# Optimization experiments

Measured on AMD Instinct MI355X. Metric: run time of the kernel, lower is better.

The kernel has to match this reference:

```python
import jax, jax.numpy as jnp
import numpy as np

H = W = 1024
CHUNK = 32  # rows per chunk in the column EDT pass (keeps intermediate at 32*H*W floats)


def setup_inputs() -> dict:
    key = jax.random.key(0)
    k1, k2 = jax.random.split(key)
    preds = jax.random.randint(k1, (H, W), 0, 2).astype(jnp.float32)
    targets = jax.random.randint(k2, (H, W), 0, 2).astype(jnp.float32)
    return {"preds": preds, "targets": targets}


def _edges(seg):
    # morphological erosion via 3x3 box conv, threshold at 9 == kernel.numel()
    s = seg[None, None]  # (1,1,H,W)
    kern = jnp.ones((1, 1, 3, 3), seg.dtype)
    conv = jax.lax.conv_general_dilated(s, kern, (1, 1), ((1, 1), (1, 1)))
    eroded = (conv[0, 0] == 9.0).astype(seg.dtype)
    return seg - eroded


def _edt(edges):
    # exact Euclidean distance transform: distance to nearest zero of (1 - edges),
    # i.e. nearest pixel where edges == 1.  Separable exact algorithm:
    #   1) per-row 1D distance to nearest feature (via cummax/cummin scans)
    #   2) per-column lower envelope min_k g2[k,j] + (i-k)^2 (chunked brute force)
    feat = (1.0 - edges) == 0.0
    Hh, Ww = edges.shape
    BIG = jnp.float32(1e6)
    col = jnp.arange(Ww, dtype=jnp.float32)
    left = col - jax.lax.cummax(jnp.where(feat, col, -BIG), axis=1)
    right = jax.lax.cummin(jnp.where(feat, col, BIG), axis=1, reverse=True) - col
    g = jnp.minimum(jnp.minimum(left, right), BIG)  # row-wise 1D distance
    g2 = g * g  # (H,W) squared row distances
    rows = jnp.arange(Hh, dtype=jnp.float32)

    def chunk(ic):  # ic: (CHUNK,) target row indices
        # (CHUNK, H, W): g2[k,j] + (i-k)^2, min over source row k
        d = g2[None, :, :] + (ic[:, None, None] - rows[None, :, None]) ** 2
        return jnp.min(d, axis=1)  # (CHUNK, W)

    D2 = jax.lax.map(chunk, rows.reshape(-1, CHUNK)).reshape(Hh, Ww)
    return jnp.sqrt(D2)


def reference(preds, targets):
    pred_edges = _edges(preds)
    target_edges = _edges(targets)
    # scipy EDT ran on detached CPU copies -> no gradient through the DTs
    pred_dt = jax.lax.stop_gradient(_edt(pred_edges))
    target_dt = jax.lax.stop_gradient(_edt(target_edges))
    pred_err = target_edges * pred_dt
    target_err = pred_edges * target_dt
    loss = (jnp.mean(pred_err) + jnp.mean(target_err)) / 2.0
    return jax.nn.sigmoid(loss)
```

## Files before the change

kernel.cpp:

```cpp
#include <hip/hip_runtime.h>
#include <hip/hip_bf16.h>
#include <math.h>


#define HW 1024
#define BIGF 1e6f
#define RMIN_SENT (1 << 30)

__global__ __launch_bounds__(256)
void k_rows(const float* __restrict__ pred, const float* __restrict__ targ,
            float* __restrict__ hp, float* __restrict__ ht,
            unsigned char* __restrict__ ep, unsigned char* __restrict__ et)
{
    const int r = blockIdx.x;
    const int m = blockIdx.y;
    const int t = threadIdx.x;
    const float* __restrict__ seg = m ? targ : pred;
    float* __restrict__ hout = m ? ht : hp;
    unsigned char* __restrict__ eout = m ? et : ep;

    __shared__ unsigned char colall[HW];
    __shared__ int wtotL[4];
    __shared__ int wtotR[4];

    const int j4 = t * 4;
    float4 c0 = *(const float4*)&seg[r * HW + j4];
    float4 cm = make_float4(0.f, 0.f, 0.f, 0.f);
    float4 cp = make_float4(0.f, 0.f, 0.f, 0.f);
    if (r > 0)        cm = *(const float4*)&seg[(r - 1) * HW + j4];
    if (r < HW - 1)   cp = *(const float4*)&seg[(r + 1) * HW + j4];

    const float s0v[4] = {c0.x, c0.y, c0.z, c0.w};
    const float smv[4] = {cm.x, cm.y, cm.z, cm.w};
    const float spv[4] = {cp.x, cp.y, cp.z, cp.w};

    unsigned char ca[4];
    #pragma unroll
    for (int u = 0; u < 4; ++u)
        ca[u] = (s0v[u] != 0.f && smv[u] != 0.f && spv[u] != 0.f) ? 1 : 0;
    *(uchar4*)&colall[j4] = make_uchar4(ca[0], ca[1], ca[2], ca[3]);
    __syncthreads();

    int lmax = -1, rmin = RMIN_SENT;
    unsigned char fe[4];
    #pragma unroll
    for (int u = 0; u < 4; ++u) {
        const int j = j4 + u;
        int er = 0;
        if (j > 0 && j < HW - 1)
            er = colall[j - 1] & ca[u] & colall[j + 1];
        const int e = (s0v[u] != 0.f) && !er;
        fe[u] = (unsigned char)e;
        if (e) { lmax = j; if (rmin == RMIN_SENT) rmin = j; }
    }
    *(uchar4*)&eout[r * HW + j4] = make_uchar4(fe[0], fe[1], fe[2], fe[3]);

    const int lane = t & 63;
    const int wv   = t >> 6;
    int Li = lmax;
    #pragma unroll
    for (int off = 1; off < 64; off <<= 1) {
        const int v = __shfl_up(Li, off);
        if (lane >= off) Li = max(Li, v);
    }
    int Ri = rmin;
    #pragma unroll
    for (int off = 1; off < 64; off <<= 1) {
        const int v = __shfl_down(Ri, off);
        if (lane + off < 64) Ri = min(Ri, v);
    }
    if (lane == 63) wtotL[wv] = Li;
    if (lane == 0)  wtotR[wv] = Ri;
    int exL = __shfl_up(Li, 1);  if (lane == 0)  exL = -1;
    int exR = __shfl_down(Ri, 1); if (lane == 63) exR = RMIN_SENT;
    __syncthreads();
    int baseL = -1, baseR = RMIN_SENT;
    #pragma unroll
    for (int w2 = 0; w2 < 4; ++w2) {
        if (w2 < wv) baseL = max(baseL, wtotL[w2]);
        if (w2 > wv) baseR = min(baseR, wtotR[w2]);
    }
    const int carryL = max(baseL, exL);
    const int carryR = min(baseR, exR);

    int Lv[4], Rv[4];
    {
        int L = carryL;
        #pragma unroll
        for (int u = 0; u < 4; ++u) { if (fe[u]) L = j4 + u; Lv[u] = L; }
    }
    {
        int R = carryR;
        #pragma unroll
        for (int u = 3; u >= 0; --u) { if (fe[u]) R = j4 + u; Rv[u] = R; }
    }

    const float rr = (float)(r * r);
    float hv[4];
    #pragma unroll
    for (int u = 0; u < 4; ++u) {
        const float jf = (float)(j4 + u);
        const float left  = jf - ((Lv[u] < 0) ? -BIGF : (float)Lv[u]);
        const float right = ((Rv[u] >= RMIN_SENT) ? BIGF : (float)Rv[u]) - jf;
        float g = fminf(fminf(left, right), BIGF);
        hv[u] = g * g + rr;
    }
    float4 ho; ho.x = hv[0]; ho.y = hv[1]; ho.z = hv[2]; ho.w = hv[3];
    *(float4*)&hout[r * HW + j4] = ho;
}

#define WIN 8
#define RPB 128
#define KROWS (RPB + 2 * WIN)
#define HS_STRIDE 17
#define NBLK 1024

__global__ __launch_bounds__(256)
void k_cols(const float* __restrict__ hp, const float* __restrict__ ht,
            const unsigned char* __restrict__ ep, const unsigned char* __restrict__ et,
            float* __restrict__ partial)
{
    const int j0 = blockIdx.x * 16;
    const int i0 = blockIdx.y * RPB;
    const int m  = blockIdx.z;
    const float* __restrict__ hg = m ? ht : hp;
    const unsigned char* __restrict__ ew = m ? ep : et;

    __shared__ float hs[KROWS * HS_STRIDE];
    __shared__ alignas(16) unsigned char es[RPB * 16];
    __shared__ float wsum[4];

    for (int idx = threadIdx.x; idx < KROWS * 16; idx += 256) {
        const int kk = idx >> 4, jc = idx & 15;
        const int gk = i0 - WIN + kk;
        float v = 1e30f;
        if ((unsigned)gk < (unsigned)HW) v = hg[gk * HW + j0 + jc];
        hs[kk * HS_STRIDE + jc] = v;
    }
    if (threadIdx.x < RPB)
        *(uint4*)&es[threadIdx.x * 16] = *(const uint4*)&ew[(i0 + threadIdx.x) * HW + j0];
    __syncthreads();

    const int jj = threadIdx.x & 15;
    const int iw = threadIdx.x >> 4;
    float lsum = 0.f;

    #pragma unroll
    for (int g = 0; g < 2; ++g) {
        const int ib = i0 + iw * 8 + g * 4;
        const int kkS = iw * 8 + g * 4;
        float b0 = 3e38f, b1 = 3e38f, b2 = 3e38f, b3 = 3e38f;
        float kf = (float)(ib - WIN);
        const float m0 = -2.f * (float)(ib);
        const float m1 = -2.f * (float)(ib + 1);
        const float m2 = -2.f * (float)(ib + 2);
        const float m3 = -2.f * (float)(ib + 3);
        #pragma unroll
        for (int kk = kkS; kk < kkS + 2 * WIN + 4; ++kk) {
            const float hvv = hs[kk * HS_STRIDE + jj];
            b0 = fminf(b0, fmaf(m0, kf, hvv));
            b1 = fminf(b1, fmaf(m1, kf, hvv));
            b2 = fminf(b2, fmaf(m2, kf, hvv));
            b3 = fminf(b3, fmaf(m3, kf, hvv));
            kf += 1.f;
        }
        const int sLo = max(0, ib - WIN);
        const int sHi = min(HW - 1, ib + WIN + 3);
        float bs[4] = {b0, b1, b2, b3};
        #pragma unroll
        for (int w = 0; w < 4; ++w) {
            const int i = ib + w;
            float D2 = (float)(i * i) + bs[w];
            const int dl = i - sLo + 1, dr = sHi + 1 - i;
            const bool need = ((sLo > 0) && (D2 > (float)(dl * dl))) ||
                              ((sHi < HW - 1) && (D2 > (float)(dr * dr)));
            if (need) {
                float bb = 3e38f, k2 = 0.f;
                const float mm = -2.f * (float)i;
                for (int k = 0; k < HW; ++k) {
                    bb = fminf(bb, fmaf(mm, k2, hg[k * HW + j0 + jj]));
                    k2 += 1.f;
                }
                D2 = (float)(i * i) + bb;
            }
            const float wgt = (float)es[(i - i0) * 16 + jj];
            lsum = fmaf(wgt, sqrtf(D2), lsum);
        }
    }

    #pragma unroll
    for (int off = 32; off > 0; off >>= 1) lsum += __shfl_down(lsum, off);
    if ((threadIdx.x & 63) == 0) wsum[threadIdx.x >> 6] = lsum;
    __syncthreads();
    if (threadIdx.x == 0) {
        const int bid = blockIdx.x + 64 * (blockIdx.y + 8 * blockIdx.z);
        partial[bid] = wsum[0] + wsum[1] + wsum[2] + wsum[3];
    }
}

__global__ __launch_bounds__(256)
void k_fin(const float* __restrict__ partial, float* __restrict__ out)
{
    const int t = threadIdx.x;
    float s = partial[t] + partial[t + 256] + partial[t + 512] + partial[t + 768];
    #pragma unroll
    for (int off = 32; off > 0; off >>= 1) s += __shfl_down(s, off);
    __shared__ float w[4];
    if ((t & 63) == 0) w[t >> 6] = s;
    __syncthreads();
    if (t == 0) {
        const float tot = w[0] + w[1] + w[2] + w[3];
        const float loss = tot * (1.f / (2.f * 1024.f * 1024.f));
        out[0] = 1.f / (1.f + expf(-loss));
    }
}

extern "C" void kernel_launch(void* const* d_in, const int* in_sizes, int n_in,
                              void* d_out, int out_size, void* d_ws, size_t ws_size,
                              hipStream_t stream)
{
    const float* preds   = (const float*)d_in[0];
    const float* targets = (const float*)d_in[1];
    float* out = (float*)d_out;

    char* ws = (char*)d_ws;
    float* hp = (float*)ws;
    float* ht = hp + HW * HW;
    unsigned char* ep = (unsigned char*)(ht + HW * HW);
    unsigned char* et = ep + HW * HW;
    float* partial = (float*)(et + HW * HW);

    dim3 gA(HW, 2, 1);
    k_rows<<<gA, 256, 0, stream>>>(preds, targets, hp, ht, ep, et);

    dim3 gB(HW / 16, HW / RPB, 2);
    k_cols<<<gB, 256, 0, stream>>>(hp, ht, ep, et, partial);

    k_fin<<<1, 256, 0, stream>>>(partial, out);
}
```

Baseline: 78.31 us.

## Fuse row, column and final reduction kernels into one cooperative persistent kernel

Merges the three separate launches into a single cooperative kernel with a fixed grid of 512 blocks that loops over row tasks, grid-syncs, loops over column tiles, grid-syncs again, and then has block 0 do the final reduction. This is meant to remove the launch overhead and inter-kernel gaps of two extra launches. In exchange it adds grid-wide barriers, persistent-loop scheduling with fewer concurrent blocks, and a launch_bounds occupancy hint, and it relies on all 512 blocks being co-resident.

```diff
diff --git a/kernel.cpp b/kernel.cpp
--- a/kernel.cpp
+++ b/kernel.cpp
@@ -1,217 +1,221 @@
 #include <hip/hip_runtime.h>
-#include <hip/hip_bf16.h>
+#include <hip/hip_cooperative_groups.h>
 #include <math.h>
+
+namespace cg = cooperative_groups;
 
 
 #define HW 1024
 #define BIGF 1e6f
 #define RMIN_SENT (1 << 30)
-
-__global__ __launch_bounds__(256)
-void k_rows(const float* __restrict__ pred, const float* __restrict__ targ,
-            float* __restrict__ hp, float* __restrict__ ht,
-            unsigned char* __restrict__ ep, unsigned char* __restrict__ et)
-{
-    const int r = blockIdx.x;
-    const int m = blockIdx.y;
-    const int t = threadIdx.x;
-    const float* __restrict__ seg = m ? targ : pred;
-    float* __restrict__ hout = m ? ht : hp;
-    unsigned char* __restrict__ eout = m ? et : ep;
-
-    __shared__ unsigned char colall[HW];
-    __shared__ int wtotL[4];
-    __shared__ int wtotR[4];
-
-    const int j4 = t * 4;
-    float4 c0 = *(const float4*)&seg[r * HW + j4];
-    float4 cm = make_float4(0.f, 0.f, 0.f, 0.f);
-    float4 cp = make_float4(0.f, 0.f, 0.f, 0.f);
-    if (r > 0)        cm = *(const float4*)&seg[(r - 1) * HW + j4];
-    if (r < HW - 1)   cp = *(const float4*)&seg[(r + 1) * HW + j4];
-
-    const float s0v[4] = {c0.x, c0.y, c0.z, c0.w};
-    const float smv[4] = {cm.x, cm.y, cm.z, cm.w};
-    const float spv[4] = {cp.x, cp.y, cp.z, cp.w};
-
-    unsigned char ca[4];
-    #pragma unroll
-    for (int u = 0; u < 4; ++u)
-        ca[u] = (s0v[u] != 0.f && smv[u] != 0.f && spv[u] != 0.f) ? 1 : 0;
-    *(uchar4*)&colall[j4] = make_uchar4(ca[0], ca[1], ca[2], ca[3]);
-    __syncthreads();
-
-    int lmax = -1, rmin = RMIN_SENT;
-    unsigned char fe[4];
-    #pragma unroll
-    for (int u = 0; u < 4; ++u) {
-        const int j = j4 + u;
-        int er = 0;
-        if (j > 0 && j < HW - 1)
-            er = colall[j - 1] & ca[u] & colall[j + 1];
-        const int e = (s0v[u] != 0.f) && !er;
-        fe[u] = (unsigned char)e;
-        if (e) { lmax = j; if (rmin == RMIN_SENT) rmin = j; }
-    }
-    *(uchar4*)&eout[r * HW + j4] = make_uchar4(fe[0], fe[1], fe[2], fe[3]);
-
-    const int lane = t & 63;
-    const int wv   = t >> 6;
-    int Li = lmax;
-    #pragma unroll
-    for (int off = 1; off < 64; off <<= 1) {
-        const int v = __shfl_up(Li, off);
-        if (lane >= off) Li = max(Li, v);
-    }
-    int Ri = rmin;
-    #pragma unroll
-    for (int off = 1; off < 64; off <<= 1) {
-        const int v = __shfl_down(Ri, off);
-        if (lane + off < 64) Ri = min(Ri, v);
-    }
-    if (lane == 63) wtotL[wv] = Li;
-    if (lane == 0)  wtotR[wv] = Ri;
-    int exL = __shfl_up(Li, 1);  if (lane == 0)  exL = -1;
-    int exR = __shfl_down(Ri, 1); if (lane == 63) exR = RMIN_SENT;
-    __syncthreads();
-    int baseL = -1, baseR = RMIN_SENT;
-    #pragma unroll
-    for (int w2 = 0; w2 < 4; ++w2) {
-        if (w2 < wv) baseL = max(baseL, wtotL[w2]);
-        if (w2 > wv) baseR = min(baseR, wtotR[w2]);
-    }
-    const int carryL = max(baseL, exL);
-    const int carryR = min(baseR, exR);
-
-    int Lv[4], Rv[4];
-    {
-        int L = carryL;
-        #pragma unroll
-        for (int u = 0; u < 4; ++u) { if (fe[u]) L = j4 + u; Lv[u] = L; }
-    }
-    {
-        int R = carryR;
-        #pragma unroll
-        for (int u = 3; u >= 0; --u) { if (fe[u]) R = j4 + u; Rv[u] = R; }
-    }
-
-    const float rr = (float)(r * r);
-    float hv[4];
-    #pragma unroll
-    for (int u = 0; u < 4; ++u) {
-        const float jf = (float)(j4 + u);
-        const float left  = jf - ((Lv[u] < 0) ? -BIGF : (float)Lv[u]);
-        const float right = ((Rv[u] >= RMIN_SENT) ? BIGF : (float)Rv[u]) - jf;
-        float g = fminf(fminf(left, right), BIGF);
-        hv[u] = g * g + rr;
-    }
-    float4 ho; ho.x = hv[0]; ho.y = hv[1]; ho.z = hv[2]; ho.w = hv[3];
-    *(float4*)&hout[r * HW + j4] = ho;
-}
-
 #define WIN 8
 #define RPB 128
 #define KROWS (RPB + 2 * WIN)
 #define HS_STRIDE 17
-#define NBLK 1024
-
-__global__ __launch_bounds__(256)
-void k_cols(const float* __restrict__ hp, const float* __restrict__ ht,
-            const unsigned char* __restrict__ ep, const unsigned char* __restrict__ et,
-            float* __restrict__ partial)
+#define GRID 512
+
+__global__ __launch_bounds__(256, 2)
+void k_fused(const float* __restrict__ pred, const float* __restrict__ targ,
+             float* __restrict__ hp, float* __restrict__ ht,
+             unsigned char* __restrict__ ep, unsigned char* __restrict__ et,
+             float* __restrict__ partial, float* __restrict__ out)
 {
-    const int j0 = blockIdx.x * 16;
-    const int i0 = blockIdx.y * RPB;
-    const int m  = blockIdx.z;
-    const float* __restrict__ hg = m ? ht : hp;
-    const unsigned char* __restrict__ ew = m ? ep : et;
-
+    __shared__ unsigned char colall[HW];
+    __shared__ int wtotL[4];
+    __shared__ int wtotR[4];
     __shared__ float hs[KROWS * HS_STRIDE];
     __shared__ alignas(16) unsigned char es[RPB * 16];
     __shared__ float wsum[4];
 
-    for (int idx = threadIdx.x; idx < KROWS * 16; idx += 256) {
-        const int kk = idx >> 4, jc = idx & 15;
-        const int gk = i0 - WIN + kk;
-        float v = 1e30f;
-        if ((unsigned)gk < (unsigned)HW) v = hg[gk * HW + j0 + jc];
-        hs[kk * HS_STRIDE + jc] = v;
+    const int t = threadIdx.x;
+    cg::grid_group grid = cg::this_grid();
+
+    for (int task = blockIdx.x; task < 2 * HW; task += GRID) {
+        const int r = task & (HW - 1);
+        const int m = task >> 10;
+        const float* __restrict__ seg = m ? targ : pred;
+        float* __restrict__ hout = m ? ht : hp;
+        unsigned char* __restrict__ eout = m ? et : ep;
+
+        const int j4 = t * 4;
+        float4 c0 = *(const float4*)&seg[r * HW + j4];
+        float4 cm = make_float4(0.f, 0.f, 0.f, 0.f);
+        float4 cp = make_float4(0.f, 0.f, 0.f, 0.f);
+        if (r > 0)        cm = *(const float4*)&seg[(r - 1) * HW + j4];
+        if (r < HW - 1)   cp = *(const float4*)&seg[(r + 1) * HW + j4];
+
+        const float s0v[4] = {c0.x, c0.y, c0.z, c0.w};
+        const float smv[4] = {cm.x, cm.y, cm.z, cm.w};
+        const float spv[4] = {cp.x, cp.y, cp.z, cp.w};
+
+        unsigned char ca[4];
+        #pragma unroll
+        for (int u = 0; u < 4; ++u)
+            ca[u] = (s0v[u] != 0.f && smv[u] != 0.f && spv[u] != 0.f) ? 1 : 0;
+        *(uchar4*)&colall[j4] = make_uchar4(ca[0], ca[1], ca[2], ca[3]);
+        __syncthreads();
+
+        int lmax = -1, rmin = RMIN_SENT;
+        unsigned char fe[4];
+        #pragma unroll
+        for (int u = 0; u < 4; ++u) {
+            const int j = j4 + u;
+            int er = 0;
+            if (j > 0 && j < HW - 1)
+                er = colall[j - 1] & ca[u] & colall[j + 1];
+            const int e = (s0v[u] != 0.f) && !er;
+            fe[u] = (unsigned char)e;
+            if (e) { lmax = j; if (rmin == RMIN_SENT) rmin = j; }
+        }
+        *(uchar4*)&eout[r * HW + j4] = make_uchar4(fe[0], fe[1], fe[2], fe[3]);
+
+        const int lane = t & 63;
+        const int wv   = t >> 6;
+        int Li = lmax;
+        #pragma unroll
+        for (int off = 1; off < 64; off <<= 1) {
+            const int v = __shfl_up(Li, off);
+            if (lane >= off) Li = max(Li, v);
+        }
+        int Ri = rmin;
+        #pragma unroll
+        for (int off = 1; off < 64; off <<= 1) {
+            const int v = __shfl_down(Ri, off);
+            if (lane + off < 64) Ri = min(Ri, v);
+        }
+        if (lane == 63) wtotL[wv] = Li;
+        if (lane == 0)  wtotR[wv] = Ri;
+        int exL = __shfl_up(Li, 1);   if (lane == 0)  exL = -1;
+        int exR = __shfl_down(Ri, 1); if (lane == 63) exR = RMIN_SENT;
+        __syncthreads();
+        int baseL = -1, baseR = RMIN_SENT;
+        #pragma unroll
+        for (int w2 = 0; w2 < 4; ++w2) {
+            if (w2 < wv) baseL = max(baseL, wtotL[w2]);
+            if (w2 > wv) baseR = min(baseR, wtotR[w2]);
+        }
+        const int carryL = max(baseL, exL);
+        const int carryR = min(baseR, exR);
+
+        int Lv[4], Rv[4];
+        {
+            int L = carryL;
+            #pragma unroll
+            for (int u = 0; u < 4; ++u) { if (fe[u]) L = j4 + u; Lv[u] = L; }
+        }
+        {
+            int R = carryR;
+            #pragma unroll
+            for (int u = 3; u >= 0; --u) { if (fe[u]) R = j4 + u; Rv[u] = R; }
+        }
+
+        const float rr = (float)(r * r);
+        float hv[4];
+        #pragma unroll
+        for (int u = 0; u < 4; ++u) {
+            const float jf = (float)(j4 + u);
+            const float left  = jf - ((Lv[u] < 0) ? -BIGF : (float)Lv[u]);
+            const float right = ((Rv[u] >= RMIN_SENT) ? BIGF : (float)Rv[u]) - jf;
+            float g = fminf(fminf(left, right), BIGF);
+            hv[u] = g * g + rr;
+        }
+        float4 ho; ho.x = hv[0]; ho.y = hv[1]; ho.z = hv[2]; ho.w = hv[3];
+        *(float4*)&hout[r * HW + j4] = ho;
     }
-    if (threadIdx.x < RPB)
-        *(uint4*)&es[threadIdx.x * 16] = *(const uint4*)&ew[(i0 + threadIdx.x) * HW + j0];
-    __syncthreads();
-
-    const int jj = threadIdx.x & 15;
-    const int iw = threadIdx.x >> 4;
-    float lsum = 0.f;
-
-    #pragma unroll
-    for (int g = 0; g < 2; ++g) {
-        const int ib = i0 + iw * 8 + g * 4;
-        const int kkS = iw * 8 + g * 4;
-        float b0 = 3e38f, b1 = 3e38f, b2 = 3e38f, b3 = 3e38f;
-        float kf = (float)(ib - WIN);
-        const float m0 = -2.f * (float)(ib);
-        const float m1 = -2.f * (float)(ib + 1);
-        const float m2 = -2.f * (float)(ib + 2);
-        const float m3 = -2.f * (float)(ib + 3);
-        #pragma unroll
-        for (int kk = kkS; kk < kkS + 2 * WIN + 4; ++kk) {
-            const float hvv = hs[kk * HS_STRIDE + jj];
-            b0 = fminf(b0, fmaf(m0, kf, hvv));
-            b1 = fminf(b1, fmaf(m1, kf, hvv));
-            b2 = fminf(b2, fmaf(m2, kf, hvv));
-            b3 = fminf(b3, fmaf(m3, kf, hvv));
-            kf += 1.f;
-        }
-        const int sLo = max(0, ib - WIN);
-        const int sHi = min(HW - 1, ib + WIN + 3);
-        float bs[4] = {b0, b1, b2, b3};
-        #pragma unroll
-        for (int w = 0; w < 4; ++w) {
-            const int i = ib + w;
-            float D2 = (float)(i * i) + bs[w];
-            const int dl = i - sLo + 1, dr = sHi + 1 - i;
-            const bool need = ((sLo > 0) && (D2 > (float)(dl * dl))) ||
-                              ((sHi < HW - 1) && (D2 > (float)(dr * dr)));
-            if (need) {
-                float bb = 3e38f, k2 = 0.f;
-                const float mm = -2.f * (float)i;
-                for (int k = 0; k < HW; ++k) {
-                    bb = fminf(bb, fmaf(mm, k2, hg[k * HW + j0 + jj]));
-                    k2 += 1.f;
+
+    __threadfence();
+    grid.sync();
+
+    for (int task = blockIdx.x; task < 1024; task += GRID) {
+        const int jt = task & 63;
+        const int it = (task >> 6) & 7;
+        const int m  = task >> 9;
+        const int j0 = jt * 16;
+        const int i0 = it * RPB;
+        const float* __restrict__ hg = m ? ht : hp;
+        const unsigned char* __restrict__ ew = m ? ep : et;
+
+        for (int idx = t; idx < KROWS * 16; idx += 256) {
+            const int kk = idx >> 4, jc = idx & 15;
+            const int gk = i0 - WIN + kk;
+            float v = 1e30f;
+            if ((unsigned)gk < (unsigned)HW) v = hg[gk * HW + j0 + jc];
+            hs[kk * HS_STRIDE + jc] = v;
+        }
+        if (t < RPB)
+            *(uint4*)&es[t * 16] = *(const uint4*)&ew[(i0 + t) * HW + j0];
+        __syncthreads();
+
+        const int jj = t & 15;
+        const int iw = t >> 4;
+        float lsum = 0.f;
+
+        #pragma unroll
+        for (int g = 0; g < 2; ++g) {
+            const int ib = i0 + iw * 8 + g * 4;
+            const int kkS = iw * 8 + g * 4;
+            float b0 = 3e38f, b1 = 3e38f, b2 = 3e38f, b3 = 3e38f;
+            float kf = (float)(ib - WIN);
+            const float m0 = -2.f * (float)(ib);
+            const float m1 = -2.f * (float)(ib + 1);
+            const float m2 = -2.f * (float)(ib + 2);
+            const float m3 = -2.f * (float)(ib + 3);
+            #pragma unroll
+            for (int kk = kkS; kk < kkS + 2 * WIN + 4; ++kk) {
+                const float hvv = hs[kk * HS_STRIDE + jj];
+                b0 = fminf(b0, fmaf(m0, kf, hvv));
+                b1 = fminf(b1, fmaf(m1, kf, hvv));
+                b2 = fminf(b2, fmaf(m2, kf, hvv));
+                b3 = fminf(b3, fmaf(m3, kf, hvv));
+                kf += 1.f;
+            }
+            const int sLo = max(0, ib - WIN);
+            const int sHi = min(HW - 1, ib + WIN + 3);
+            float bs[4] = {b0, b1, b2, b3};
+            #pragma unroll
+            for (int w = 0; w < 4; ++w) {
+                const int i = ib + w;
+                float D2 = (float)(i * i) + bs[w];
+                const int dl = i - sLo + 1, dr = sHi + 1 - i;
+                const bool need = ((sLo > 0) && (D2 > (float)(dl * dl))) ||
+                                  ((sHi < HW - 1) && (D2 > (float)(dr * dr)));
+                if (need) {
+                    float bb = 3e38f, k2 = 0.f;
+                    const float mm = -2.f * (float)i;
+                    for (int k = 0; k < HW; ++k) {
+                        bb = fminf(bb, fmaf(mm, k2, hg[k * HW + j0 + jj]));
+                        k2 += 1.f;
+                    }
+                    D2 = (float)(i * i) + bb;
                 }
-                D2 = (float)(i * i) + bb;
+                const float wgt = (float)es[(i - i0) * 16 + jj];
+                lsum = fmaf(wgt, sqrtf(D2), lsum);
             }
-            const float wgt = (float)es[(i - i0) * 16 + jj];
-            lsum = fmaf(wgt, sqrtf(D2), lsum);
-        }
+        }
+
+        #pragma unroll
+        for (int off = 32; off > 0; off >>= 1) lsum += __shfl_down(lsum, off);
+        if ((t & 63) == 0) wsum[t >> 6] = lsum;
+        __syncthreads();
+        if (t == 0)
+            partial[task] = wsum[0] + wsum[1] + wsum[2] + wsum[3];
+        __syncthreads();
     }
 
-    #pragma unroll
-    for (int off = 32; off > 0; off >>= 1) lsum += __shfl_down(lsum, off);
-    if ((threadIdx.x & 63) == 0) wsum[threadIdx.x >> 6] = lsum;
-    __syncthreads();
-    if (threadIdx.x == 0) {
-        const int bid = blockIdx.x + 64 * (blockIdx.y + 8 * blockIdx.z);
-        partial[bid] = wsum[0] + wsum[1] + wsum[2] + wsum[3];
-    }
-}
-
-__global__ __launch_bounds__(256)
-void k_fin(const float* __restrict__ partial, float* __restrict__ out)
-{
-    const int t = threadIdx.x;
-    float s = partial[t] + partial[t + 256] + partial[t + 512] + partial[t + 768];
-    #pragma unroll
-    for (int off = 32; off > 0; off >>= 1) s += __shfl_down(s, off);
-    __shared__ float w[4];
-    if ((t & 63) == 0) w[t >> 6] = s;
-    __syncthreads();
-    if (t == 0) {
-        const float tot = w[0] + w[1] + w[2] + w[3];
-        const float loss = tot * (1.f / (2.f * 1024.f * 1024.f));
-        out[0] = 1.f / (1.f + expf(-loss));
+    __threadfence();
+    grid.sync();
+
+    if (blockIdx.x == 0) {
+        float s = partial[t] + partial[t + 256] + partial[t + 512] + partial[t + 768];
+        #pragma unroll
+        for (int off = 32; off > 0; off >>= 1) s += __shfl_down(s, off);
+        if ((t & 63) == 0) wsum[t >> 6] = s;
+        __syncthreads();
+        if (t == 0) {
+            const float tot = wsum[0] + wsum[1] + wsum[2] + wsum[3];
+            const float loss = tot * (1.f / (2.f * 1024.f * 1024.f));
+            out[0] = 1.f / (1.f + expf(-loss));
+        }
     }
 }
 
@@ -230,11 +234,8 @@
     unsigned char* et = ep + HW * HW;
     float* partial = (float*)(et + HW * HW);
 
-    dim3 gA(HW, 2, 1);
-    k_rows<<<gA, 256, 0, stream>>>(preds, targets, hp, ht, ep, et);
-
-    dim3 gB(HW / 16, HW / RPB, 2);
-    k_cols<<<gB, 256, 0, stream>>>(hp, ht, ep, et, partial);
-
-    k_fin<<<1, 256, 0, stream>>>(partial, out);
+    void* args[] = { (void*)&preds, (void*)&targets, (void*)&hp, (void*)&ht,
+                     (void*)&ep, (void*)&et, (void*)&partial, (void*)&out };
+    hipLaunchCooperativeKernel((const void*)k_fused, dim3(GRID), dim3(256),
+                               args, 0, stream);
 }
```

Result: slower. 277.9 us (+254.8%).

## Process one row per wavefront in row pass using bitmask erosion

Applied to the files above, without the earlier changes.

The row kernel now maps each row to a single 64-lane wavefront, with each lane handling 16 columns. Erosion and the nearest-edge search are done with 16-bit masks, clz/ffs and shuffles, replacing the shared-memory column buffer, the cross-wave scan and both __syncthreads. This removes block-level synchronisation and shared-memory traffic from the row pass. In exchange each lane holds more registers and issues scattered 16-float loads per row.

```diff
diff --git a/kernel.cpp b/kernel.cpp
--- a/kernel.cpp
+++ b/kernel.cpp
@@ -1,5 +1,4 @@
 #include <hip/hip_runtime.h>
-#include <hip/hip_bf16.h>
 #include <math.h>
 
 
@@ -12,108 +11,109 @@
             float* __restrict__ hp, float* __restrict__ ht,
             unsigned char* __restrict__ ep, unsigned char* __restrict__ et)
 {
-    const int r = blockIdx.x;
-    const int m = blockIdx.y;
-    const int t = threadIdx.x;
+    const int t    = threadIdx.x;
+    const int lane = t & 63;
+    const int wv   = t >> 6;
+    const int r    = blockIdx.x * 4 + wv;
+    const int m    = blockIdx.y;
     const float* __restrict__ seg = m ? targ : pred;
     float* __restrict__ hout = m ? ht : hp;
     unsigned char* __restrict__ eout = m ? et : ep;
 
-    __shared__ unsigned char colall[HW];
-    __shared__ int wtotL[4];
-    __shared__ int wtotR[4];
-
-    const int j4 = t * 4;
-    float4 c0 = *(const float4*)&seg[r * HW + j4];
-    float4 cm = make_float4(0.f, 0.f, 0.f, 0.f);
-    float4 cp = make_float4(0.f, 0.f, 0.f, 0.f);
-    if (r > 0)        cm = *(const float4*)&seg[(r - 1) * HW + j4];
-    if (r < HW - 1)   cp = *(const float4*)&seg[(r + 1) * HW + j4];
-
-    const float s0v[4] = {c0.x, c0.y, c0.z, c0.w};
-    const float smv[4] = {cm.x, cm.y, cm.z, cm.w};
-    const float spv[4] = {cp.x, cp.y, cp.z, cp.w};
-
-    unsigned char ca[4];
-    #pragma unroll
-    for (int u = 0; u < 4; ++u)
-        ca[u] = (s0v[u] != 0.f && smv[u] != 0.f && spv[u] != 0.f) ? 1 : 0;
-    *(uchar4*)&colall[j4] = make_uchar4(ca[0], ca[1], ca[2], ca[3]);
-    __syncthreads();
-
-    int lmax = -1, rmin = RMIN_SENT;
-    unsigned char fe[4];
-    #pragma unroll
-    for (int u = 0; u < 4; ++u) {
-        const int j = j4 + u;
-        int er = 0;
-        if (j > 0 && j < HW - 1)
-            er = colall[j - 1] & ca[u] & colall[j + 1];
-        const int e = (s0v[u] != 0.f) && !er;
-        fe[u] = (unsigned char)e;
-        if (e) { lmax = j; if (rmin == RMIN_SENT) rmin = j; }
-    }
-    *(uchar4*)&eout[r * HW + j4] = make_uchar4(fe[0], fe[1], fe[2], fe[3]);
-
-    const int lane = t & 63;
-    const int wv   = t >> 6;
-    int Li = lmax;
+    const int c0 = lane * 16;
+
+    float cs[16], cm[16], cp[16];
+    #pragma unroll
+    for (int q = 0; q < 4; ++q)
+        *(float4*)&cs[q * 4] = *(const float4*)&seg[r * HW + c0 + q * 4];
+    #pragma unroll
+    for (int q = 0; q < 4; ++q) {
+        *(float4*)&cm[q * 4] = make_float4(0.f, 0.f, 0.f, 0.f);
+        *(float4*)&cp[q * 4] = make_float4(0.f, 0.f, 0.f, 0.f);
+    }
+    if (r > 0) {
+        #pragma unroll
+        for (int q = 0; q < 4; ++q)
+            *(float4*)&cm[q * 4] = *(const float4*)&seg[(r - 1) * HW + c0 + q * 4];
+    }
+    if (r < HW - 1) {
+        #pragma unroll
+        for (int q = 0; q < 4; ++q)
+            *(float4*)&cp[q * 4] = *(const float4*)&seg[(r + 1) * HW + c0 + q * 4];
+    }
+
+    unsigned s_bits = 0, va_bits = 0;
+    #pragma unroll
+    for (int x = 0; x < 16; ++x) {
+        const unsigned s  = (cs[x] != 0.f) ? 1u : 0u;
+        const unsigned va = (cs[x] != 0.f && cm[x] != 0.f && cp[x] != 0.f) ? 1u : 0u;
+        s_bits  |= s  << x;
+        va_bits |= va << x;
+    }
+
+    const unsigned vprev = __shfl_up(va_bits, 1);
+    const unsigned vnext = __shfl_down(va_bits, 1);
+    const unsigned lbit = (lane == 0)  ? 0u : ((vprev >> 15) & 1u);
+    const unsigned rbit = (lane == 63) ? 0u : (vnext & 1u);
+
+    const unsigned w18 = (va_bits << 1) | lbit | (rbit << 17);
+    const unsigned eroded = w18 & (w18 >> 1) & (w18 >> 2);
+    const unsigned edge = s_bits & ~eroded & 0xFFFFu;
+
+    uint4 eb;
+    unsigned ew[4];
+    #pragma unroll
+    for (int q = 0; q < 4; ++q) {
+        unsigned u = 0;
+        #pragma unroll
+        for (int b = 0; b < 4; ++b)
+            u |= ((edge >> (q * 4 + b)) & 1u) << (8 * b);
+        ew[q] = u;
+    }
+    eb.x = ew[0]; eb.y = ew[1]; eb.z = ew[2]; eb.w = ew[3];
+    *(uint4*)&eout[r * HW + c0] = eb;
+
+    const int lane_last  = edge ? (c0 + 31 - __clz(edge)) : -1;
+    const int lane_first = edge ? (c0 + __ffs(edge) - 1)  : RMIN_SENT;
+
+    int Li = lane_last;
     #pragma unroll
     for (int off = 1; off < 64; off <<= 1) {
         const int v = __shfl_up(Li, off);
         if (lane >= off) Li = max(Li, v);
     }
-    int Ri = rmin;
+    int Ri = lane_first;
     #pragma unroll
     for (int off = 1; off < 64; off <<= 1) {
         const int v = __shfl_down(Ri, off);
         if (lane + off < 64) Ri = min(Ri, v);
     }
-    if (lane == 63) wtotL[wv] = Li;
-    if (lane == 0)  wtotR[wv] = Ri;
-    int exL = __shfl_up(Li, 1);  if (lane == 0)  exL = -1;
-    int exR = __shfl_down(Ri, 1); if (lane == 63) exR = RMIN_SENT;
-    __syncthreads();
-    int baseL = -1, baseR = RMIN_SENT;
-    #pragma unroll
-    for (int w2 = 0; w2 < 4; ++w2) {
-        if (w2 < wv) baseL = max(baseL, wtotL[w2]);
-        if (w2 > wv) baseR = min(baseR, wtotR[w2]);
-    }
-    const int carryL = max(baseL, exL);
-    const int carryR = min(baseR, exR);
-
-    int Lv[4], Rv[4];
-    {
-        int L = carryL;
-        #pragma unroll
-        for (int u = 0; u < 4; ++u) { if (fe[u]) L = j4 + u; Lv[u] = L; }
-    }
-    {
-        int R = carryR;
-        #pragma unroll
-        for (int u = 3; u >= 0; --u) { if (fe[u]) R = j4 + u; Rv[u] = R; }
-    }
+    int carryL = __shfl_up(Li, 1);   if (lane == 0)  carryL = -1;
+    int carryR = __shfl_down(Ri, 1); if (lane == 63) carryR = RMIN_SENT;
 
     const float rr = (float)(r * r);
-    float hv[4];
-    #pragma unroll
-    for (int u = 0; u < 4; ++u) {
-        const float jf = (float)(j4 + u);
-        const float left  = jf - ((Lv[u] < 0) ? -BIGF : (float)Lv[u]);
-        const float right = ((Rv[u] >= RMIN_SENT) ? BIGF : (float)Rv[u]) - jf;
-        float g = fminf(fminf(left, right), BIGF);
-        hv[u] = g * g + rr;
-    }
-    float4 ho; ho.x = hv[0]; ho.y = hv[1]; ho.z = hv[2]; ho.w = hv[3];
-    *(float4*)&hout[r * HW + j4] = ho;
+    float hv[16];
+    #pragma unroll
+    for (int x = 0; x < 16; ++x) {
+        const unsigned ble = edge & ((2u << x) - 1u);
+        const int L = ble ? (c0 + 31 - __clz(ble)) : carryL;
+        const unsigned bge = edge >> x;
+        const int R = bge ? (c0 + x + __ffs(bge) - 1) : carryR;
+        const float jf = (float)(c0 + x);
+        const float left  = jf - ((L < 0) ? -BIGF : (float)L);
+        const float right = ((R >= RMIN_SENT) ? BIGF : (float)R) - jf;
+        const float g = fminf(fminf(left, right), BIGF);
+        hv[x] = g * g + rr;
+    }
+    #pragma unroll
+    for (int q = 0; q < 4; ++q)
+        *(float4*)&hout[r * HW + c0 + q * 4] = *(float4*)&hv[q * 4];
 }
 
 #define WIN 8
 #define RPB 128
 #define KROWS (RPB + 2 * WIN)
 #define HS_STRIDE 17
-#define NBLK 1024
 
 __global__ __launch_bounds__(256)
 void k_cols(const float* __restrict__ hp, const float* __restrict__ ht,
@@ -230,7 +230,7 @@
     unsigned char* et = ep + HW * HW;
     float* partial = (float*)(et + HW * HW);
 
-    dim3 gA(HW, 2, 1);
+    dim3 gA(HW / 4, 2, 1);
     k_rows<<<gA, 256, 0, stream>>>(preds, targets, hp, ht, ep, et);
 
     dim3 gB(HW / 16, HW / RPB, 2);
```

Result: no change. 77.13 us (-1.5%).
